# Optimization experiments

Hardware: AMD Instinct MI355X
Metric: run time of the kernel (lower is better)

## Reference

```python
import jax, jax.numpy as jnp
import numpy as np

MIN_N = 4
MAX_N = 5
MIN_FREQ = 2 ** MIN_N  # 16
DT = 0.005
W = 1.0e6
HUBER = 0.005
N0 = 5
EPS_VAR = 1e-6


def _skew(v):
    x, y, z = v[..., 0], v[..., 1], v[..., 2]
    o = jnp.zeros_like(x)
    return jnp.stack([
        jnp.stack([o, -z, y], -1),
        jnp.stack([z, o, -x], -1),
        jnp.stack([-y, x, o], -1)], -2)


def so3_exp(phi):
    """Rodrigues formula: axis-angle (M,3) -> rotation matrices (M,3,3)."""
    a2 = jnp.sum(phi * phi, axis=-1)
    small = a2 < 1e-12
    a2s = jnp.where(small, 1.0, a2)
    a = jnp.sqrt(a2s)
    sin_t = jnp.where(small, 1.0 - a2 / 6.0, jnp.sin(a) / a)
    cos_t = jnp.where(small, 0.5 - a2 / 24.0, (1.0 - jnp.cos(a)) / a2s)
    Wm = _skew(phi)
    I = jnp.eye(3, dtype=phi.dtype)
    return I + sin_t[..., None, None] * Wm + cos_t[..., None, None] * jnp.matmul(Wm, Wm)


def so3_log(R):
    """Rotation matrices (M,3,3) -> axis-angle (M,3)."""
    tr = R[..., 0, 0] + R[..., 1, 1] + R[..., 2, 2]
    cos = jnp.clip(0.5 * (tr - 1.0), -1.0 + 1e-6, 1.0 - 1e-6)
    angle = jnp.arccos(cos)
    small = angle < 1e-6
    factor = jnp.where(small, 0.5, angle / (2.0 * jnp.sin(jnp.where(small, 1.0, angle))))
    # vee(R - R^T)
    w = jnp.stack([R[..., 2, 1] - R[..., 1, 2],
                   R[..., 0, 2] - R[..., 2, 0],
                   R[..., 1, 0] - R[..., 0, 1]], -1)
    return factor[..., None] * w


def _smooth_l1_mean(x):
    ax = jnp.abs(x)
    return jnp.mean(jnp.where(ax < 1.0, 0.5 * ax * ax, ax - 0.5))


def _f_huber(rs):
    return W * _smooth_l1_mean(rs / HUBER) * HUBER ** 2


def _pairwise(R):
    # drot[::2] @ drot[1::2]
    return jnp.matmul(R[::2], R[1::2])


def _bmtm_log(A, B):
    # SO3.log(A^T B)
    return so3_log(jnp.einsum('nij,nik->njk', A, B))


def setup_inputs() -> dict:
    key = jax.random.key(0)
    ks = jax.random.split(key, 5)
    N, T = 128, 16384
    return {
        'w_hat': jax.random.normal(ks[0], (N, T, 3), jnp.float32),
        'dw_16': jax.random.normal(ks[1], (N, T, 3), jnp.float32),
        'w_gt': jax.random.normal(ks[2], (N, T, 3), jnp.float32),
        'w_mean': jax.random.normal(ks[3], (N, T, 3), jnp.float32),
        'w_std': jax.random.uniform(ks[4], (N, T, 3), jnp.float32),
    }


def reference(w_hat, dw_16, w_gt, w_mean, w_std):
    N = dw_16.shape[0]
    # --- gyro loss ---
    drot_16 = so3_exp(dw_16[:, ::MIN_FREQ].reshape(-1, 3))
    drot_hat = so3_exp(DT * w_hat.reshape(-1, 3))
    for _ in range(MIN_N):
        drot_hat = _pairwise(drot_hat)
    rs = _bmtm_log(drot_hat, drot_16).reshape(N, -1, 3)[:, N0:]
    gyro16 = _f_huber(rs)
    gyro32 = jnp.zeros((), rs.dtype)
    for k in range(MIN_N, MAX_N):
        drot_hat = _pairwise(drot_hat)
        drot_16 = _pairwise(drot_16)
        rs = _bmtm_log(drot_hat, drot_16).reshape(N, -1, 3)[:, N0:]
        gyro32 = _f_huber(rs) / 2 ** (k - MIN_N + 1) / 2.0
    # --- gaussian NLL ---
    w_var = w_std ** 2
    w_var = jnp.where(w_var < EPS_VAR, EPS_VAR, w_var)
    gap = w_gt - w_hat
    gnll = jnp.mean((jnp.log(w_var) + (gap - w_mean) ** 2 / w_var) / 2.0)
    return gyro16 + gyro32 + gnll
```

## Files before the change

### kernel.cpp

```cpp
#include <hip/hip_runtime.h>

#define THREADS 256
#define NROWS 2097152
#define BLOCKS (NROWS / THREADS)
#define DT 0.005f
#define INV_HUBER 200.0f

#define NELEM 6291456.0
#define CNT16 391296.0
#define CNT32 194688.0

__device__ __forceinline__ void so3_exp3(float x, float y, float z, float R[9]) {
    float a2 = x * x + y * y + z * z;
    bool sm = a2 < 1e-12f;
    float a2s = sm ? 1.0f : a2;
    float a = sqrtf(a2s);
    float s = sinf(a);
    float c = cosf(a);
    float st = sm ? (1.0f - a2 * (1.0f / 6.0f)) : (s / a);
    float ct = sm ? (0.5f - a2 * (1.0f / 24.0f)) : ((1.0f - c) / a2s);
    R[0] = 1.0f + ct * (x * x - a2);
    R[1] = ct * (x * y) - st * z;
    R[2] = ct * (x * z) + st * y;
    R[3] = ct * (x * y) + st * z;
    R[4] = 1.0f + ct * (y * y - a2);
    R[5] = ct * (y * z) - st * x;
    R[6] = ct * (x * z) - st * y;
    R[7] = ct * (y * z) + st * x;
    R[8] = 1.0f + ct * (z * z - a2);
}

__device__ __forceinline__ void mm3(const float A[9], const float B[9], float C[9]) {
#pragma unroll
    for (int i = 0; i < 3; ++i) {
        float a0 = A[3 * i], a1 = A[3 * i + 1], a2 = A[3 * i + 2];
        C[3 * i + 0] = a0 * B[0] + a1 * B[3] + a2 * B[6];
        C[3 * i + 1] = a0 * B[1] + a1 * B[4] + a2 * B[7];
        C[3 * i + 2] = a0 * B[2] + a1 * B[5] + a2 * B[8];
    }
}

__device__ __forceinline__ float huber_bmtm(const float A[9], const float B[9]) {
    float tr = 0.f, w0 = 0.f, w1 = 0.f, w2 = 0.f;
#pragma unroll
    for (int k = 0; k < 3; ++k) {
        float a0 = A[3 * k], a1 = A[3 * k + 1], a2v = A[3 * k + 2];
        float b0 = B[3 * k], b1 = B[3 * k + 1], b2v = B[3 * k + 2];
        tr += a0 * b0 + a1 * b1 + a2v * b2v;
        w0 += a2v * b1 - a1 * b2v;
        w1 += a0 * b2v - a2v * b0;
        w2 += a1 * b0 - a0 * b1;
    }
    float cs = 0.5f * (tr - 1.0f);
    cs = fminf(fmaxf(cs, -1.0f + 1e-6f), 1.0f - 1e-6f);
    float ang = acosf(cs);
    float sn = sqrtf(fmaxf(1.0f - cs * cs, 0.0f));
    float fac = ang / (2.0f * sn);
    float h = 0.0f, r;
    r = fabsf(fac * w0 * INV_HUBER); h += (r < 1.0f) ? 0.5f * r * r : (r - 0.5f);
    r = fabsf(fac * w1 * INV_HUBER); h += (r < 1.0f) ? 0.5f * r * r : (r - 0.5f);
    r = fabsf(fac * w2 * INV_HUBER); h += (r < 1.0f) ? 0.5f * r * r : (r - 0.5f);
    return h;
}

__global__ __launch_bounds__(THREADS) void dg_loss_kernel(
    const float* __restrict__ w_hat, const float* __restrict__ dw16,
    const float* __restrict__ w_gt, const float* __restrict__ w_mean,
    const float* __restrict__ w_std, double* __restrict__ partial)
{
    const int r = blockIdx.x * THREADS + threadIdx.x;
    const int lane = threadIdx.x & 63;

    const size_t o = (size_t)r * 3;
    const float h0 = w_hat[o], h1 = w_hat[o + 1], h2 = w_hat[o + 2];
    const float g0 = w_gt[o], g1 = w_gt[o + 1], g2 = w_gt[o + 2];
    const float m0 = w_mean[o], m1 = w_mean[o + 1], m2 = w_mean[o + 2];
    const float s0 = w_std[o], s1 = w_std[o + 1], s2 = w_std[o + 2];

    double lg;
    {
        float v = fmaxf(s0 * s0, 1e-6f); float d = g0 - h0 - m0;
        float p = logf(v) + d * d / v;
        v = fmaxf(s1 * s1, 1e-6f); d = g1 - h1 - m1;
        p += logf(v) + d * d / v;
        v = fmaxf(s2 * s2, 1e-6f); d = g2 - h2 - m2;
        p += logf(v) + d * d / v;
        lg = 0.5 * (double)p;
    }

    float P[9];
    so3_exp3(DT * h0, DT * h1, DT * h2, P);
#pragma unroll
    for (int s = 1; s <= 8; s <<= 1) {
        float Nb[9];
#pragma unroll
        for (int e = 0; e < 9; ++e) Nb[e] = __shfl_xor(P[e], s);
        const bool rt = (lane & s) != 0;
        float A[9], B[9], T[9];
#pragma unroll
        for (int e = 0; e < 9; ++e) { A[e] = rt ? Nb[e] : P[e]; B[e] = rt ? P[e] : Nb[e]; }
        mm3(A, B, T);
#pragma unroll
        for (int e = 0; e < 9; ++e) P[e] = T[e];
    }

    const int b = r >> 4;
    const size_t qo = (size_t)b * 48;
    float Q[9];
    {
        const float q0 = dw16[qo], q1 = dw16[qo + 1], q2 = dw16[qo + 2];
        so3_exp3(q0, q1, q2, Q);
    }

    double lh16 = 0.0, lh32 = 0.0;
    const int sub = lane & 15;
    if (sub == 0 && ((b & 1023) >= 5))
        lh16 = (double)huber_bmtm(P, Q);

    float Pn[9], Qn[9];
#pragma unroll
    for (int e = 0; e < 9; ++e) {
        Pn[e] = __shfl_xor(P[e], 16);
        Qn[e] = __shfl_xor(Q[e], 16);
    }
    if ((lane & 31) == 0) {
        const int c = r >> 5;
        if ((c & 511) >= 5) {
            float P32[9], Q32[9];
            mm3(P, Pn, P32);
            mm3(Q, Qn, Q32);
            lh32 = (double)huber_bmtm(P32, Q32);
        }
    }

    double part = lg * (1.0 / NELEM) + lh16 * (25.0 / CNT16) + lh32 * (6.25 / CNT32);
    __shared__ double s_p[4];
#pragma unroll
    for (int off = 32; off > 0; off >>= 1)
        part += __shfl_down(part, off);
    const int wv = threadIdx.x >> 6;
    if (lane == 0) s_p[wv] = part;
    __syncthreads();
    if (threadIdx.x == 0)
        partial[blockIdx.x] = s_p[0] + s_p[1] + s_p[2] + s_p[3];
}

__global__ __launch_bounds__(THREADS) void finalize_kernel(
    const double* __restrict__ partial, float* __restrict__ out)
{
    double s = 0.0;
#pragma unroll
    for (int i = 0; i < BLOCKS / THREADS; ++i)
        s += partial[i * THREADS + threadIdx.x];
    __shared__ double s_p[4];
#pragma unroll
    for (int off = 32; off > 0; off >>= 1)
        s += __shfl_down(s, off);
    const int lane = threadIdx.x & 63, wv = threadIdx.x >> 6;
    if (lane == 0) s_p[wv] = s;
    __syncthreads();
    if (threadIdx.x == 0)
        out[0] = (float)(s_p[0] + s_p[1] + s_p[2] + s_p[3]);
}

extern "C" void kernel_launch(void* const* d_in, const int* in_sizes, int n_in,
                              void* d_out, int out_size, void* d_ws, size_t ws_size,
                              hipStream_t stream) {
    const float* w_hat = (const float*)d_in[0];
    const float* dw16 = (const float*)d_in[1];
    const float* w_gt = (const float*)d_in[2];
    const float* w_mean = (const float*)d_in[3];
    const float* w_std = (const float*)d_in[4];
    float* out = (float*)d_out;
    double* partial = (double*)d_ws;

    dg_loss_kernel<<<BLOCKS, THREADS, 0, stream>>>(
        w_hat, dw16, w_gt, w_mean, w_std, partial);
    finalize_kernel<<<1, THREADS, 0, stream>>>(partial, out);
}
```

Baseline: 162.5 us.

## Coarsen to four rows per thread with float4 loads and Taylor SO3 exp

```diff
diff --git a/kernel.cpp b/kernel.cpp
--- a/kernel.cpp
+++ b/kernel.cpp
@@ -1,8 +1,8 @@
 #include <hip/hip_runtime.h>
 
 #define THREADS 256
-#define NROWS 2097152
-#define BLOCKS (NROWS / THREADS)
+#define NQUAD 524288
+#define BLOCKS (NQUAD / THREADS)
 #define DT 0.005f
 #define INV_HUBER 200.0f
 
@@ -10,13 +10,28 @@
 #define CNT16 391296.0
 #define CNT32 194688.0
 
-__device__ __forceinline__ void so3_exp3(float x, float y, float z, float R[9]) {
+__device__ __forceinline__ void so3_exp_small(float x, float y, float z, float R[9]) {
+    float a2 = x * x + y * y + z * z;
+    float st = 1.0f - a2 * (1.0f / 6.0f) * (1.0f - a2 * (1.0f / 20.0f));
+    float ct = 0.5f - a2 * (1.0f / 24.0f) * (1.0f - a2 * (1.0f / 30.0f));
+    R[0] = 1.0f + ct * (x * x - a2);
+    R[1] = ct * (x * y) - st * z;
+    R[2] = ct * (x * z) + st * y;
+    R[3] = ct * (x * y) + st * z;
+    R[4] = 1.0f + ct * (y * y - a2);
+    R[5] = ct * (y * z) - st * x;
+    R[6] = ct * (x * z) - st * y;
+    R[7] = ct * (y * z) + st * x;
+    R[8] = 1.0f + ct * (z * z - a2);
+}
+
+__device__ __forceinline__ void so3_exp_full(float x, float y, float z, float R[9]) {
     float a2 = x * x + y * y + z * z;
     bool sm = a2 < 1e-12f;
     float a2s = sm ? 1.0f : a2;
     float a = sqrtf(a2s);
-    float s = sinf(a);
-    float c = cosf(a);
+    float s, c;
+    sincosf(a, &s, &c);
     float st = sm ? (1.0f - a2 * (1.0f / 6.0f)) : (s / a);
     float ct = sm ? (0.5f - a2 * (1.0f / 24.0f)) : ((1.0f - c) / a2s);
     R[0] = 1.0f + ct * (x * x - a2);
@@ -63,35 +78,53 @@
     return h;
 }
 
+__device__ __forceinline__ float gnll4(float4 h, float4 g, float4 m, float4 s) {
+    float p = 0.f;
+#pragma unroll
+    for (int k = 0; k < 4; ++k) {
+        float hv = (&h.x)[k], gv = (&g.x)[k], mv = (&m.x)[k], sv = (&s.x)[k];
+        float v = fmaxf(sv * sv, 1e-6f);
+        float d = gv - hv - mv;
+        float rv = __builtin_amdgcn_rcpf(v);
+        rv = rv * (2.0f - v * rv);
+        p += __logf(v) + d * d * rv;
+    }
+    return p;
+}
+
 __global__ __launch_bounds__(THREADS) void dg_loss_kernel(
     const float* __restrict__ w_hat, const float* __restrict__ dw16,
     const float* __restrict__ w_gt, const float* __restrict__ w_mean,
     const float* __restrict__ w_std, double* __restrict__ partial)
 {
-    const int r = blockIdx.x * THREADS + threadIdx.x;
+    const int t = blockIdx.x * THREADS + threadIdx.x;
     const int lane = threadIdx.x & 63;
 
-    const size_t o = (size_t)r * 3;
-    const float h0 = w_hat[o], h1 = w_hat[o + 1], h2 = w_hat[o + 2];
-    const float g0 = w_gt[o], g1 = w_gt[o + 1], g2 = w_gt[o + 2];
-    const float m0 = w_mean[o], m1 = w_mean[o + 1], m2 = w_mean[o + 2];
-    const float s0 = w_std[o], s1 = w_std[o + 1], s2 = w_std[o + 2];
-
-    double lg;
-    {
-        float v = fmaxf(s0 * s0, 1e-6f); float d = g0 - h0 - m0;
-        float p = logf(v) + d * d / v;
-        v = fmaxf(s1 * s1, 1e-6f); d = g1 - h1 - m1;
-        p += logf(v) + d * d / v;
-        v = fmaxf(s2 * s2, 1e-6f); d = g2 - h2 - m2;
-        p += logf(v) + d * d / v;
-        lg = 0.5 * (double)p;
-    }
-
-    float P[9];
-    so3_exp3(DT * h0, DT * h1, DT * h2, P);
-#pragma unroll
-    for (int s = 1; s <= 8; s <<= 1) {
+    const float4* hp = (const float4*)w_hat + (size_t)t * 3;
+    const float4* gp = (const float4*)w_gt + (size_t)t * 3;
+    const float4* mp = (const float4*)w_mean + (size_t)t * 3;
+    const float4* sp = (const float4*)w_std + (size_t)t * 3;
+    const int b = t >> 2;
+    float4 q4 = ((const float4*)dw16)[(size_t)b * 12];
+
+    float4 h0 = hp[0], h1 = hp[1], h2 = hp[2];
+    float4 g0 = gp[0], g1 = gp[1], g2 = gp[2];
+    float4 m0 = mp[0], m1 = mp[1], m2 = mp[2];
+    float4 s0 = sp[0], s1 = sp[1], s2 = sp[2];
+
+    double lg = 0.5 * (double)(gnll4(h0, g0, m0, s0) + gnll4(h1, g1, m1, s1) + gnll4(h2, g2, m2, s2));
+
+    float E0[9], E1[9], E2[9], E3[9], T01[9], T23[9], P[9];
+    so3_exp_small(DT * h0.x, DT * h0.y, DT * h0.z, E0);
+    so3_exp_small(DT * h0.w, DT * h1.x, DT * h1.y, E1);
+    so3_exp_small(DT * h1.z, DT * h1.w, DT * h2.x, E2);
+    so3_exp_small(DT * h2.y, DT * h2.z, DT * h2.w, E3);
+    mm3(E0, E1, T01);
+    mm3(E2, E3, T23);
+    mm3(T01, T23, P);
+
+#pragma unroll
+    for (int s = 1; s <= 2; s <<= 1) {
         float Nb[9];
 #pragma unroll
         for (int e = 0; e < 9; ++e) Nb[e] = __shfl_xor(P[e], s);
@@ -104,27 +137,21 @@
         for (int e = 0; e < 9; ++e) P[e] = T[e];
     }
 
-    const int b = r >> 4;
-    const size_t qo = (size_t)b * 48;
     float Q[9];
-    {
-        const float q0 = dw16[qo], q1 = dw16[qo + 1], q2 = dw16[qo + 2];
-        so3_exp3(q0, q1, q2, Q);
-    }
+    so3_exp_full(q4.x, q4.y, q4.z, Q);
 
     double lh16 = 0.0, lh32 = 0.0;
-    const int sub = lane & 15;
-    if (sub == 0 && ((b & 1023) >= 5))
+    if ((lane & 3) == 0 && ((b & 1023) >= 5))
         lh16 = (double)huber_bmtm(P, Q);
 
     float Pn[9], Qn[9];
 #pragma unroll
     for (int e = 0; e < 9; ++e) {
-        Pn[e] = __shfl_xor(P[e], 16);
-        Qn[e] = __shfl_xor(Q[e], 16);
-    }
-    if ((lane & 31) == 0) {
-        const int c = r >> 5;
+        Pn[e] = __shfl_xor(P[e], 4);
+        Qn[e] = __shfl_xor(Q[e], 4);
+    }
+    if ((lane & 7) == 0) {
+        const int c = t >> 3;
         if ((c & 511) >= 5) {
             float P32[9], Q32[9];
             mm3(P, Pn, P32);
```

Result: faster. 146.6 us (-9.8%).
